# Kernel tuning notes

Measured on AMD Instinct MI355X. Metric: run time of the kernel, lower is better.

Reference implementation:

```python
import jax, jax.numpy as jnp
import numpy as np

N, E, D, B, C = 50000, 800000, 128, 20000, 40
EPS_BN = 1e-3    # keras BatchNormalization default epsilon
EPS_NRM = 1e-12  # keras ops.nn.normalize epsilon
FFN_DIMS = {"pre": (D, D), "c1p": (D, D), "c1u": (2 * D, D), "c2p": (D, D), "c2u": (2 * D, D), "post": (D, D)}


def setup_inputs() -> dict:
    key = jax.random.key(0)
    ks = jax.random.split(key, 8)
    inp = {
        "node_features": jax.random.normal(ks[0], (N, D), jnp.float32),
        "edges": jax.random.randint(ks[1], (2, E), 0, N, dtype=jnp.int32),
        "edge_w": jax.random.uniform(ks[2], (E,), jnp.float32),
        "input_node_idx": jax.random.randint(ks[3], (B,), 0, N, dtype=jnp.int32),
    }
    for i, (name, (din, dout)) in enumerate(FFN_DIMS.items()):
        kw = jax.random.fold_in(key, 100 + i)
        inp[name + "_g"] = jnp.ones((din,), jnp.float32)
        inp[name + "_be"] = jnp.zeros((din,), jnp.float32)
        inp[name + "_mu"] = jnp.zeros((din,), jnp.float32)
        inp[name + "_var"] = jnp.ones((din,), jnp.float32)
        inp[name + "_w"] = jax.random.normal(kw, (din, dout), jnp.float32) * (1.0 / float(np.sqrt(din)))
        inp[name + "_bi"] = jnp.zeros((dout,), jnp.float32)
    inp["logits_w"] = jax.random.normal(ks[4], (D, C), jnp.float32) * (1.0 / float(np.sqrt(D)))
    inp["logits_b"] = jnp.zeros((C,), jnp.float32)
    return inp


def ffn(x, g, be, mu, var, w, bi):
    # BatchNorm (inference running stats) -> Dropout (identity) -> Dense + exact gelu
    xn = (x - mu) * jax.lax.rsqrt(var + EPS_BN) * g + be
    return jax.nn.gelu(xn @ w + bi, approximate=False)


def l2norm(x):
    n = jnp.sqrt(jnp.sum(x * x, axis=-1, keepdims=True))
    return x / jnp.maximum(n, EPS_NRM)


def graph_conv(x, node_idx, nbr_idx, ew, prep, upd):
    # gather neighbours -> prepare FFN -> edge-weighted -> segment_sum (reduce='sum')
    msgs = ffn(x[nbr_idx], *prep) * ew[:, None]                         # [E, D]
    red = jax.ops.segment_sum(msgs, node_idx, num_segments=x.shape[0])  # [N, D]
    h = jnp.concatenate([x, red], axis=1)                               # [N, 2D] (combination='concat')
    return l2norm(ffn(h, *upd))                                         # normalize=True


def reference(node_features, edges, edge_w, input_node_idx,
              pre_g, pre_be, pre_mu, pre_var, pre_w, pre_bi,
              c1p_g, c1p_be, c1p_mu, c1p_var, c1p_w, c1p_bi,
              c1u_g, c1u_be, c1u_mu, c1u_var, c1u_w, c1u_bi,
              c2p_g, c2p_be, c2p_mu, c2p_var, c2p_w, c2p_bi,
              c2u_g, c2u_be, c2u_mu, c2u_var, c2u_w, c2u_bi,
              post_g, post_be, post_mu, post_var, post_w, post_bi,
              logits_w, logits_b):
    ew = edge_w / jnp.sum(edge_w)                       # edge_W normalized at init
    node_idx, nbr_idx = edges[0], edges[1]
    x = ffn(node_features, pre_g, pre_be, pre_mu, pre_var, pre_w, pre_bi)
    x = graph_conv(x, node_idx, nbr_idx, ew,
                   (c1p_g, c1p_be, c1p_mu, c1p_var, c1p_w, c1p_bi),
                   (c1u_g, c1u_be, c1u_mu, c1u_var, c1u_w, c1u_bi)) + x
    x = graph_conv(x, node_idx, nbr_idx, ew,
                   (c2p_g, c2p_be, c2p_mu, c2p_var, c2p_w, c2p_bi),
                   (c2u_g, c2u_be, c2u_mu, c2u_var, c2u_w, c2u_bi)) + x
    x = ffn(x, post_g, post_be, post_mu, post_var, post_w, post_bi)
    return x[input_node_idx] @ logits_w + logits_b      # [B, C]
```

## Files before the change

### kernel.cpp

```cpp
#include <hip/hip_runtime.h>
#include <hip/hip_fp16.h>
#include <math.h>

static constexpr int D = 128;
static constexpr int CAP = 64;
static constexpr float EPS_BN = 1e-3f;

typedef short short8 __attribute__((ext_vector_type(8)));
typedef short short4v __attribute__((ext_vector_type(4)));
typedef float float4v __attribute__((ext_vector_type(4)));

__device__ __forceinline__ float gelu_exact(float x) {
    return 0.5f * x * (1.0f + erff(x * 0.70710678118654752f));
}

__device__ __forceinline__ void f32_to_hilo(float f, short& h, short& l) {
    unsigned u = __float_as_uint(f);
    h = (short)(u >> 16);
    float hf = __uint_as_float(u & 0xFFFF0000u);
    unsigned lu = __float_as_uint(f - hf);
    l = (short)(lu >> 16);
}

__device__ __forceinline__ short f32_to_bf16_rne(float f) {
    unsigned u = __float_as_uint(f);
    u += 0x7FFFu + ((u >> 16) & 1u);
    return (short)(u >> 16);
}

__device__ __forceinline__ void cvt_hilo8(const float4& x, const float4& y, short8& h8, short8& l8) {
    short h, l;
    f32_to_hilo(x.x, h, l); h8[0] = h; l8[0] = l;
    f32_to_hilo(x.y, h, l); h8[1] = h; l8[1] = l;
    f32_to_hilo(x.z, h, l); h8[2] = h; l8[2] = l;
    f32_to_hilo(x.w, h, l); h8[3] = h; l8[3] = l;
    f32_to_hilo(y.x, h, l); h8[4] = h; l8[4] = l;
    f32_to_hilo(y.y, h, l); h8[5] = h; l8[5] = l;
    f32_to_hilo(y.z, h, l); h8[6] = h; l8[6] = l;
    f32_to_hilo(y.w, h, l); h8[7] = h; l8[7] = l;
}

__device__ __forceinline__ short8 cvt_rne8(const float4& x, const float4& y) {
    short8 r;
    r[0] = f32_to_bf16_rne(x.x); r[1] = f32_to_bf16_rne(x.y);
    r[2] = f32_to_bf16_rne(x.z); r[3] = f32_to_bf16_rne(x.w);
    r[4] = f32_to_bf16_rne(y.x); r[5] = f32_to_bf16_rne(y.y);
    r[6] = f32_to_bf16_rne(y.z); r[7] = f32_to_bf16_rne(y.w);
    return r;
}

struct FoldArgs {
    const float* g[6]; const float* be[6]; const float* mu[6];
    const float* var[6]; const float* w[6]; const float* bi[6];
    short* wh[6]; short* wl[6]; float* bp[6]; int K[6];
};

__global__ void k_build(const int* __restrict__ edges, const float* __restrict__ ew,
                        int* __restrict__ cnt, float* __restrict__ sums,
                        unsigned* __restrict__ cw, FoldArgs fa, int E, int N, int fillBlocks) {
    __shared__ float sm[4];
    const int tid = threadIdx.x;
    const int lane = tid & 63, wvi = tid >> 6;

    if ((int)blockIdx.x < fillBlocks) {
        const int g = blockIdx.x & 7;
        const int bid = blockIdx.x >> 3;
        const int gstride = (fillBlocks >> 3) * 256;
        const int N8 = (N + 7) >> 3;
        const int lo = g * N8;
        const int hi = min(lo + N8, N);
        float s = 0.f;
        for (int e = bid * 256 + tid; e < E; e += gstride) {
            int dst = edges[e];
            if (dst >= lo && dst < hi) {
                int src = edges[E + e];
                float w = ew[e];
                s += w;
                unsigned short wb = __half_as_ushort(__float2half(w));
                int idx = atomicAdd(&cnt[dst], 1);
                if (idx < CAP)
                    cw[(size_t)dst * CAP + idx] = ((unsigned)src << 16) | (unsigned)wb;
            }
        }
        for (int off = 32; off > 0; off >>= 1) s += __shfl_down(s, off, 64);
        if (lane == 0) sm[wvi] = s;
        __syncthreads();
        if (tid == 0) {
            float t = sm[0] + sm[1] + sm[2] + sm[3];
            if (t != 0.f) atomicAdd(sums, t);
        }
    } else {
        const int idx = blockIdx.x - fillBlocks;
        const int f = idx >> 7;
        const int c = idx & 127;
        const int K = fa.K[f];
        const float* g = fa.g[f]; const float* be = fa.be[f];
        const float* mu = fa.mu[f]; const float* var = fa.var[f];
        const float* w = fa.w[f]; const float* bi = fa.bi[f];
        short* wh = fa.wh[f]; short* wl = fa.wl[f]; float* bp = fa.bp[f];
        float part = 0.f;
        for (int k = tid; k < K; k += blockDim.x) {
            float a = g[k] / sqrtf(var[k] + EPS_BN);
            float wv = w[k * D + c];
            float prod = a * wv;
            short hh, ll;
            f32_to_hilo(prod, hh, ll);
            wh[c * K + k] = hh;
            wl[c * K + k] = ll;
            part += (be[k] - mu[k] * a) * wv;
        }
        for (int off = 32; off > 0; off >>= 1) part += __shfl_down(part, off, 64);
        if (lane == 0) sm[wvi] = part;
        __syncthreads();
        if (tid == 0) bp[c] = bi[c] + sm[0] + sm[1] + sm[2] + sm[3];
    }
}

__global__ void k_reduce(const int* __restrict__ cnt, const unsigned* __restrict__ cw,
                         const float* __restrict__ sums, const __half* __restrict__ y,
                         float* __restrict__ red, int N) {
    int n = blockIdx.x * (blockDim.x >> 6) + (threadIdx.x >> 6);
    if (n >= N) return;
    float inv = 1.0f / sums[0];
    int lane = threadIdx.x & 63;
    int sub = lane >> 4;
    int q = lane & 15;
    int count = min(cnt[n], CAP);
    int start = n * CAP;
    int end = start + count;
    float acc[8] = {0.f, 0.f, 0.f, 0.f, 0.f, 0.f, 0.f, 0.f};
    int i = start + sub;
    if (i < end) {
        unsigned c = cw[i];
        for (;;) {
            int ni = i + 4;
            unsigned nc = 0;
            if (ni < end) nc = cw[ni];
            int src = (int)(c >> 16);
            float w = __half2float(__ushort_as_half((unsigned short)(c & 0xFFFFu))) * inv;
            float4 raw = *((const float4*)(y + (size_t)src * D) + q);
            const __half2* hp = (const __half2*)&raw;
            #pragma unroll
            for (int t = 0; t < 4; t++) {
                float2 f = __half22float2(hp[t]);
                acc[t * 2]     += w * f.x;
                acc[t * 2 + 1] += w * f.y;
            }
            if (ni >= end) break;
            i = ni; c = nc;
        }
    }
    #pragma unroll
    for (int t = 0; t < 8; t++) {
        acc[t] += __shfl_xor(acc[t], 16, 64);
        acc[t] += __shfl_xor(acc[t], 32, 64);
    }
    if (sub == 0) {
        float4 o0 = {acc[0], acc[1], acc[2], acc[3]};
        float4 o1 = {acc[4], acc[5], acc[6], acc[7]};
        *((float4*)(red + (size_t)n * D + q * 8)) = o0;
        *((float4*)(red + (size_t)n * D + q * 8 + 4)) = o1;
    }
}

template<int K, bool SPLIT3, bool L2RES, bool OUT16>
__global__ void __launch_bounds__(512) k_ffn(
    const float* __restrict__ A0, const float* __restrict__ A1,
    const short* __restrict__ Wh, const short* __restrict__ Wl,
    const float* __restrict__ bp, const float* __restrict__ resid,
    float* __restrict__ outf, __half* __restrict__ outh, int N)
{
    constexpr int NB = SPLIT3 ? 2 : 1;
    constexpr int WSZ = 128 * K;
    constexpr int NC = K / 64;
    __shared__ short Wlds[NB * WSZ];
    __shared__ float rsum[2][16][4];

    const int tid = threadIdx.x;

    constexpr int ITER = (NB * WSZ) / (512 * 8);
    #pragma unroll
    for (int it = 0; it < ITER; ++it) {
        int s = it * 4096 + tid * 8;
        int buf = s / WSZ;
        int rem = s - buf * WSZ;
        int c = rem / K;
        int kk = (rem & (K - 1)) ^ ((c & 7) << 3);
        const short* src = (buf ? Wl : Wh) + c * K + kk;
        *(short8*)&Wlds[s] = *(const short8*)src;
    }
    __syncthreads();

    const int lane = tid & 63;
    const int wv = tid >> 6;
    const int ssub = wv >> 2;
    const int wc = wv & 3;
    const int m = lane & 15;
    const int quad = lane >> 4;
    const int nstrips = (N + 15) >> 4;
    const int stride = gridDim.x * 2;
    const int base = blockIdx.x * 2 + ssub;

    auto body = [&](int strip, bool active) {
        int r = active ? strip * 16 + m : m;
        if (r >= N) r = N - 1;
        const float* pA0 = A0 + (size_t)r * D;
        const float* pA1 = (K == 256) ? (A1 + (size_t)r * D) : pA0;

        float4 a[2][4];
        {
            const float4* s4 = (const float4*)pA0 + quad * 2;
            a[0][0] = s4[0]; a[0][1] = s4[1]; a[0][2] = s4[8]; a[0][3] = s4[9];
        }
        {
            const float4* s4 = (const float4*)(pA0 + 64) + quad * 2;
            a[1][0] = s4[0]; a[1][1] = s4[1]; a[1][2] = s4[8]; a[1][3] = s4[9];
        }

        float4v acc[2];
        acc[0] = (float4v){0.f, 0.f, 0.f, 0.f};
        acc[1] = (float4v){0.f, 0.f, 0.f, 0.f};

        #pragma unroll
        for (int cc = 0; cc < NC; ++cc) {
            #pragma unroll
            for (int ks = 0; ks < 2; ++ks) {
                const int kk = cc * 64 + ks * 32 + quad * 8;
                short8 ah, al;
                if (SPLIT3) cvt_hilo8(a[cc & 1][ks * 2], a[cc & 1][ks * 2 + 1], ah, al);
                else        ah = cvt_rne8(a[cc & 1][ks * 2], a[cc & 1][ks * 2 + 1]);
                #pragma unroll
                for (int tj = 0; tj < 2; ++tj) {
                    const int c = wc * 32 + tj * 16 + m;
                    const int idx = c * K + (kk ^ ((c & 7) << 3));
                    short8 bh = *(const short8*)&Wlds[idx];
                    if (SPLIT3) {
                        short8 bl = *(const short8*)&Wlds[WSZ + idx];
                        acc[tj] = __builtin_amdgcn_mfma_f32_16x16x32_bf16(al, bh, acc[tj], 0, 0, 0);
                        acc[tj] = __builtin_amdgcn_mfma_f32_16x16x32_bf16(ah, bl, acc[tj], 0, 0, 0);
                    }
                    acc[tj] = __builtin_amdgcn_mfma_f32_16x16x32_bf16(ah, bh, acc[tj], 0, 0, 0);
                }
            }
            if (cc + 2 < NC) {
                const int n2 = cc + 2;
                const float* src = (K == 256 && n2 >= 2) ? pA1 : pA0;
                const int kb = (K == 256) ? ((n2 & 1) * 64) : (n2 * 64);
                const float4* s4 = (const float4*)(src + kb) + quad * 2;
                a[cc & 1][0] = s4[0]; a[cc & 1][1] = s4[1];
                a[cc & 1][2] = s4[8]; a[cc & 1][3] = s4[9];
            }
        }

        #pragma unroll
        for (int tj = 0; tj < 2; ++tj) {
            float bv = bp[wc * 32 + tj * 16 + m];
            #pragma unroll
            for (int r4 = 0; r4 < 4; ++r4)
                acc[tj][r4] = gelu_exact(acc[tj][r4] + bv);
        }

        if (L2RES) {
            float ss[4];
            #pragma unroll
            for (int r4 = 0; r4 < 4; ++r4) {
                float v = acc[0][r4] * acc[0][r4] + acc[1][r4] * acc[1][r4];
                v += __shfl_xor(v, 1, 64);
                v += __shfl_xor(v, 2, 64);
                v += __shfl_xor(v, 4, 64);
                v += __shfl_xor(v, 8, 64);
                ss[r4] = v;
            }
            if (m == 0) {
                #pragma unroll
                for (int r4 = 0; r4 < 4; ++r4) rsum[ssub][quad * 4 + r4][wc] = ss[r4];
            }
            __syncthreads();
            #pragma unroll
            for (int r4 = 0; r4 < 4; ++r4) {
                const int rib = quad * 4 + r4;
                float tot = rsum[ssub][rib][0] + rsum[ssub][rib][1]
                          + rsum[ssub][rib][2] + rsum[ssub][rib][3];
                float inv = 1.0f / fmaxf(sqrtf(tot), 1e-12f);
                int row = strip * 16 + rib;
                if (active && row < N) {
                    #pragma unroll
                    for (int tj = 0; tj < 2; ++tj) {
                        int col = wc * 32 + tj * 16 + m;
                        outf[(size_t)row * D + col] = acc[tj][r4] * inv + resid[(size_t)row * D + col];
                    }
                }
            }
            __syncthreads();
        } else {
            #pragma unroll
            for (int r4 = 0; r4 < 4; ++r4) {
                int row = strip * 16 + quad * 4 + r4;
                if (active && row < N) {
                    #pragma unroll
                    for (int tj = 0; tj < 2; ++tj) {
                        int col = wc * 32 + tj * 16 + m;
                        if (OUT16) outh[(size_t)row * D + col] = __float2half(acc[tj][r4]);
                        else       outf[(size_t)row * D + col] = acc[tj][r4];
                    }
                }
            }
        }
    };

    if (L2RES) {
        int rem = nstrips - blockIdx.x * 2;
        int nit = rem > 0 ? (rem + stride - 1) / stride : 0;
        for (int it = 0; it < nit; ++it) {
            int strip = base + it * stride;
            body(strip, strip < nstrips);
        }
    } else {
        for (int strip = base; strip < nstrips; strip += stride)
            body(strip, true);
    }
}

__global__ void k_logits(const float* __restrict__ x, const int* __restrict__ idx,
                         const float* __restrict__ LW, const float* __restrict__ lb,
                         float* __restrict__ out, int B) {
    int wid = blockIdx.x * 4 + (threadIdx.x >> 6);
    int lane = threadIdx.x & 63;
    if (wid >= B) return;
    int row = __builtin_amdgcn_readfirstlane(idx[wid]);
    if (lane >= 40) return;
    float acc = lb[lane];
    const float4* xr = (const float4*)(x + (size_t)row * D);
    #pragma unroll 4
    for (int k4 = 0; k4 < 32; k4++) {
        float4 xv = xr[k4];
        acc += xv.x * LW[(4 * k4 + 0) * 40 + lane];
        acc += xv.y * LW[(4 * k4 + 1) * 40 + lane];
        acc += xv.z * LW[(4 * k4 + 2) * 40 + lane];
        acc += xv.w * LW[(4 * k4 + 3) * 40 + lane];
    }
    out[(size_t)wid * 40 + lane] = acc;
}

extern "C" void kernel_launch(void* const* d_in, const int* in_sizes, int n_in,
                              void* d_out, int out_size, void* d_ws, size_t ws_size,
                              hipStream_t stream) {
    const float* node_features = (const float*)d_in[0];
    const int*   edges         = (const int*)d_in[1];
    const float* edge_w        = (const float*)d_in[2];
    const int*   input_idx     = (const int*)d_in[3];
    const int N = in_sizes[0] / D;
    const int E = in_sizes[2];
    const int B = in_sizes[3];

    const float* P[6][6];
    for (int f = 0; f < 6; f++)
        for (int q = 0; q < 6; q++)
            P[f][q] = (const float*)d_in[4 + f * 6 + q];
    const float* logits_w = (const float*)d_in[40];
    const float* logits_b = (const float*)d_in[41];

    float* ws = (float*)d_ws;
    size_t nd = (size_t)N * D;
    float* xA  = ws;
    float* y   = ws + nd;
    float* red = ws + 2 * nd;
    float* p   = ws + 3 * nd;
    __half* yh = (__half*)p; p += nd / 2;
    const int Ks[6] = {128, 128, 256, 128, 256, 128};
    short* Wh[6]; short* Wl[6]; float* Bp[6];
    {
        short* sp = (short*)p;
        for (int f = 0; f < 6; f++) {
            Wh[f] = sp; sp += (size_t)Ks[f] * D;
            Wl[f] = sp; sp += (size_t)Ks[f] * D;
        }
        p = (float*)sp;
    }
    for (int f = 0; f < 6; f++) { Bp[f] = p; p += D; }
    int* cnt    = (int*)p; p += N;
    float* sums = p; p += 2;
    unsigned* cw = (unsigned*)p; p += (size_t)N * CAP;

    FoldArgs fa;
    for (int f = 0; f < 6; f++) {
        fa.g[f] = P[f][0]; fa.be[f] = P[f][1]; fa.mu[f] = P[f][2];
        fa.var[f] = P[f][3]; fa.w[f] = P[f][4]; fa.bi[f] = P[f][5];
        fa.wh[f] = Wh[f]; fa.wl[f] = Wl[f]; fa.bp[f] = Bp[f]; fa.K[f] = Ks[f];
    }

    const int fillBlocks = 1024;
    hipMemsetAsync(cnt, 0, ((size_t)N + 2) * sizeof(int), stream);
    k_build<<<fillBlocks + 768, 256, 0, stream>>>(edges, edge_w, cnt, sums, cw, fa, E, N, fillBlocks);

    const int rb = (N + 3) / 4;
    const int g1 = 256;
    const int g2 = 512;

    k_ffn<128, true,  false, false><<<g2, 512, 0, stream>>>(node_features, nullptr, Wh[0], Wl[0], Bp[0], nullptr, xA, nullptr, N);
    k_ffn<128, false, false, true ><<<g2, 512, 0, stream>>>(xA, nullptr, Wh[1], Wl[1], Bp[1], nullptr, nullptr, yh, N);
    k_reduce<<<rb, 256, 0, stream>>>(cnt, cw, sums, yh, red, N);
    k_ffn<256, true,  true,  false><<<g1, 512, 0, stream>>>(xA, red, Wh[2], Wl[2], Bp[2], xA, y, nullptr, N);
    k_ffn<128, false, false, true ><<<g2, 512, 0, stream>>>(y, nullptr, Wh[3], Wl[3], Bp[3], nullptr, nullptr, yh, N);
    k_reduce<<<rb, 256, 0, stream>>>(cnt, cw, sums, yh, red, N);
    k_ffn<256, true,  true,  false><<<g1, 512, 0, stream>>>(y, red, Wh[4], Wl[4], Bp[4], y, xA, nullptr, N);
    k_ffn<128, true,  false, false><<<g2, 512, 0, stream>>>(xA, nullptr, Wh[5], Wl[5], Bp[5], nullptr, red, nullptr, N);
    k_logits<<<(B + 3) / 4, 256, 0, stream>>>(red, input_idx, logits_w, logits_b, (float*)d_out, B);
}
```

Before: 449.0 us.

## Unroll neighbor gather 4x and drop dst-range partitioning in CSR build

The reduce kernel now issues four independent neighbor-row gathers per iteration before accumulating, which raises memory-level parallelism on the random fp16 row loads. The build kernel stops having each of eight block groups scan all edges and keep only a dst range; every edge is now processed exactly once. This cuts edge reads in the fill phase but loses whatever cache locality the per-range atomics and writes had. The unrolled gather also uses more registers per thread.

```diff
diff --git a/kernel.cpp b/kernel.cpp
--- a/kernel.cpp
+++ b/kernel.cpp
@@ -63,24 +63,17 @@
     const int lane = tid & 63, wvi = tid >> 6;
 
     if ((int)blockIdx.x < fillBlocks) {
-        const int g = blockIdx.x & 7;
-        const int bid = blockIdx.x >> 3;
-        const int gstride = (fillBlocks >> 3) * 256;
-        const int N8 = (N + 7) >> 3;
-        const int lo = g * N8;
-        const int hi = min(lo + N8, N);
+        const int gstride = fillBlocks * 256;
         float s = 0.f;
-        for (int e = bid * 256 + tid; e < E; e += gstride) {
+        for (int e = blockIdx.x * 256 + tid; e < E; e += gstride) {
             int dst = edges[e];
-            if (dst >= lo && dst < hi) {
-                int src = edges[E + e];
-                float w = ew[e];
-                s += w;
-                unsigned short wb = __half_as_ushort(__float2half(w));
-                int idx = atomicAdd(&cnt[dst], 1);
-                if (idx < CAP)
-                    cw[(size_t)dst * CAP + idx] = ((unsigned)src << 16) | (unsigned)wb;
-            }
+            int src = edges[E + e];
+            float w = ew[e];
+            s += w;
+            unsigned short wb = __half_as_ushort(__float2half(w));
+            int idx = atomicAdd(&cnt[dst], 1);
+            if (idx < CAP)
+                cw[(size_t)dst * CAP + idx] = ((unsigned)src << 16) | (unsigned)wb;
         }
         for (int off = 32; off > 0; off >>= 1) s += __shfl_down(s, off, 64);
         if (lane == 0) sm[wvi] = s;
@@ -116,6 +109,16 @@
     }
 }
 
+__device__ __forceinline__ void accum8(float* acc, const float4& raw, float w) {
+    const __half2* hp = (const __half2*)&raw;
+    #pragma unroll
+    for (int t = 0; t < 4; t++) {
+        float2 f = __half22float2(hp[t]);
+        acc[t * 2]     += w * f.x;
+        acc[t * 2 + 1] += w * f.y;
+    }
+}
+
 __global__ void k_reduce(const int* __restrict__ cnt, const unsigned* __restrict__ cw,
                          const float* __restrict__ sums, const __half* __restrict__ y,
                          float* __restrict__ red, int N) {
@@ -130,25 +133,29 @@
     int end = start + count;
     float acc[8] = {0.f, 0.f, 0.f, 0.f, 0.f, 0.f, 0.f, 0.f};
     int i = start + sub;
-    if (i < end) {
+    for (; i + 12 < end; i += 16) {
+        unsigned c0 = cw[i];
+        unsigned c1 = cw[i + 4];
+        unsigned c2 = cw[i + 8];
+        unsigned c3 = cw[i + 12];
+        float4 r0 = *((const float4*)(y + (size_t)(c0 >> 16) * D) + q);
+        float4 r1 = *((const float4*)(y + (size_t)(c1 >> 16) * D) + q);
+        float4 r2 = *((const float4*)(y + (size_t)(c2 >> 16) * D) + q);
+        float4 r3 = *((const float4*)(y + (size_t)(c3 >> 16) * D) + q);
+        float w0 = __half2float(__ushort_as_half((unsigned short)(c0 & 0xFFFFu))) * inv;
+        float w1 = __half2float(__ushort_as_half((unsigned short)(c1 & 0xFFFFu))) * inv;
+        float w2 = __half2float(__ushort_as_half((unsigned short)(c2 & 0xFFFFu))) * inv;
+        float w3 = __half2float(__ushort_as_half((unsigned short)(c3 & 0xFFFFu))) * inv;
+        accum8(acc, r0, w0);
+        accum8(acc, r1, w1);
+        accum8(acc, r2, w2);
+        accum8(acc, r3, w3);
+    }
+    for (; i < end; i += 4) {
         unsigned c = cw[i];
-        for (;;) {
-            int ni = i + 4;
-            unsigned nc = 0;
-            if (ni < end) nc = cw[ni];
-            int src = (int)(c >> 16);
-            float w = __half2float(__ushort_as_half((unsigned short)(c & 0xFFFFu))) * inv;
-            float4 raw = *((const float4*)(y + (size_t)src * D) + q);
-            const __half2* hp = (const __half2*)&raw;
-            #pragma unroll
-            for (int t = 0; t < 4; t++) {
-                float2 f = __half22float2(hp[t]);
-                acc[t * 2]     += w * f.x;
-                acc[t * 2 + 1] += w * f.y;
-            }
-            if (ni >= end) break;
-            i = ni; c = nc;
-        }
+        float4 r = *((const float4*)(y + (size_t)(c >> 16) * D) + q);
+        float w = __half2float(__ushort_as_half((unsigned short)(c & 0xFFFFu))) * inv;
+        accum8(acc, r, w);
     }
     #pragma unroll
     for (int t = 0; t < 8; t++) {
```

Result: no change. 450.5 us (+0.3%).
